# Kernel tuning notes

Measured on AMD Instinct MI355X. Metric: run time of the kernel, lower is better.

Reference implementation:

```python
import jax, jax.numpy as jnp
import numpy as np

ALPHA = 0.2  # leaky relu slope
NEG_BIG = -9e15


def setup_inputs() -> dict:
    key = jax.random.key(0)
    k1, k2, k3, k4 = jax.random.split(key, 4)
    B, N, Fin, Fout = 8, 2048, 128, 128
    h = jax.random.normal(k1, (B, N, Fin), dtype=jnp.float32)
    adj = jax.random.randint(k2, (N, N), 0, 2, dtype=jnp.int32)
    # xavier_uniform with gain=1.414
    limW = 1.414 * np.sqrt(6.0 / (Fin + Fout))
    W = jax.random.uniform(k3, (Fin, Fout), minval=-limW, maxval=limW, dtype=jnp.float32)
    lima = 1.414 * np.sqrt(6.0 / (2 * Fout + 1))
    a = jax.random.uniform(k4, (2 * Fout, 1), minval=-lima, maxval=lima, dtype=jnp.float32)
    return {"h": h, "adj": adj, "W": W, "a": a}


def reference(h, adj, W, a):
    # Wh: [B, N, F]
    Wh = jnp.einsum("bnf,fo->bno", h, W)
    Fout = W.shape[1]
    a1, a2 = a[:Fout, 0], a[Fout:, 0]  # [F], [F]
    # Additive score decomposition (same math as concat trick):
    # e[b,i,j] = leakyrelu(Wh_i . a1 + Wh_j . a2)
    s1 = Wh @ a1  # [B, N] (source/query part)
    s2 = Wh @ a2  # [B, N] (target part)
    e = s1[:, :, None] + s2[:, None, :]  # [B, N, N]
    e = jnp.where(e > 0, e, ALPHA * e)   # leaky relu
    e = jnp.where(adj[None, :, :] > 0, e, NEG_BIG)
    attention = jax.nn.softmax(e, axis=2)  # [B, N, N]
    # dropout is identity in eval mode
    h_prime = jnp.einsum("bij,bjf->bif", attention, Wh)
    return h_prime
```

## Files before the change

### kernel.cpp

```cpp
#include <hip/hip_runtime.h>
#include <hip/hip_bf16.h>
#include <stdint.h>

#define ALPHA 0.2f

typedef __attribute__((ext_vector_type(8))) short bf16x8;
typedef __attribute__((ext_vector_type(4))) float f32x4;

__device__ __forceinline__ short f2bf(float f) {
    union { float f; uint32_t u; } c; c.f = f;
    uint32_t u = c.u + 0x7FFF + ((c.u >> 16) & 1);
    return (short)(u >> 16);
}

__device__ __forceinline__ uint32_t pk_bf16(float lo, float hi) {
    union { float f; uint32_t u; } a, b;
    a.f = lo; b.f = hi;
    return __builtin_amdgcn_perm(b.u + 0x8000u, a.u + 0x8000u, 0x07060302u);
}

__device__ __forceinline__ void gload_lds16(const void* g, void* l) {
    __builtin_amdgcn_global_load_lds(
        (const __attribute__((address_space(1))) void*)g,
        (__attribute__((address_space(3))) void*)l, 16, 0, 0);
}

__global__ __launch_bounds__(256) void pack_adj_kernel(
        const int* __restrict__ adj, uint8_t* __restrict__ bytes,
        const float* __restrict__ W, short* __restrict__ WTg) {
    int t = blockIdx.x * 256 + threadIdx.x;
    const int4* a4 = reinterpret_cast<const int4*>(adj) + (size_t)t * 2;
    int4 x0 = a4[0], x1 = a4[1];
    uint32_t m = 0;
    m |= (x0.x > 0) ? 1u   : 0u;  m |= (x0.y > 0) ? 2u   : 0u;
    m |= (x0.z > 0) ? 4u   : 0u;  m |= (x0.w > 0) ? 8u   : 0u;
    m |= (x1.x > 0) ? 16u  : 0u;  m |= (x1.y > 0) ? 32u  : 0u;
    m |= (x1.z > 0) ? 64u  : 0u;  m |= (x1.w > 0) ? 128u : 0u;
    bytes[t] = (uint8_t)m;

    if (blockIdx.x < 64) {
        int idx = blockIdx.x * 256 + threadIdx.x;
        int k = idx >> 7, f = idx & 127;
        WTg[f * 128 + k] = f2bf(W[k * 128 + f]);
    }
}

__global__ __launch_bounds__(256) void wh_kernel(
        const float* __restrict__ h, const short* __restrict__ WTg,
        const float* __restrict__ a, short* __restrict__ whT,
        float* __restrict__ s1g, float* __restrict__ s2g) {
    __shared__ float sred[4][2][16];
    __shared__ short tr[4][32][24];

    int tid = threadIdx.x, wid = tid >> 6, lane = tid & 63;
    int q = lane >> 4, n = lane & 15;
    int bb = blockIdx.x & 7;
    int tile = blockIdx.x >> 3;
    int rb = bb * 2048 + tile * 16;
    int row = rb + n;

    f32x4 acc[2] = {};
    #pragma unroll
    for (int kc = 0; kc < 4; ++kc) {
        const float* hp = h + (size_t)row * 128 + kc * 32 + q * 8;
        float4 h0 = reinterpret_cast<const float4*>(hp)[0];
        float4 h1 = reinterpret_cast<const float4*>(hp)[1];
        bf16x8 afrag;
        afrag[0] = f2bf(h0.x); afrag[1] = f2bf(h0.y);
        afrag[2] = f2bf(h0.z); afrag[3] = f2bf(h0.w);
        afrag[4] = f2bf(h1.x); afrag[5] = f2bf(h1.y);
        afrag[6] = f2bf(h1.z); afrag[7] = f2bf(h1.w);
        #pragma unroll
        for (int u = 0; u < 2; ++u) {
            int t = wid * 2 + u;
            bf16x8 bfrag = *reinterpret_cast<const bf16x8*>(
                WTg + (t * 16 + n) * 128 + kc * 32 + q * 8);
            acc[u] = __builtin_amdgcn_mfma_f32_16x16x32_bf16(afrag, bfrag, acc[u], 0, 0, 0);
        }
    }

    float p1[4] = {0.f, 0.f, 0.f, 0.f}, p2[4] = {0.f, 0.f, 0.f, 0.f};
    #pragma unroll
    for (int u = 0; u < 2; ++u) {
        int c = (wid * 2 + u) * 16 + n;
        float a1c = a[c] * 1.442695041f;
        float a2c = a[128 + c] * 1.442695041f;
        #pragma unroll
        for (int r = 0; r < 4; ++r) {
            p1[r] += acc[u][r] * a1c;
            p2[r] += acc[u][r] * a2c;
        }
    }
    #pragma unroll
    for (int d = 1; d < 16; d <<= 1) {
        #pragma unroll
        for (int r = 0; r < 4; ++r) {
            p1[r] += __shfl_xor(p1[r], d);
            p2[r] += __shfl_xor(p2[r], d);
        }
    }
    if (n == 0) {
        #pragma unroll
        for (int r = 0; r < 4; ++r) {
            sred[wid][0][q * 4 + r] = p1[r];
            sred[wid][1][q * 4 + r] = p2[r];
        }
    }

    #pragma unroll
    for (int u = 0; u < 2; ++u)
        #pragma unroll
        for (int r = 0; r < 4; ++r)
            tr[wid][u * 16 + n][q * 4 + r] = f2bf(acc[u][r]);
    __syncthreads();

    if (wid == 0 && lane < 16) {
        float v1 = 0.f, v2 = 0.f;
        #pragma unroll
        for (int v = 0; v < 4; ++v) { v1 += sred[v][0][lane]; v2 += sred[v][1][lane]; }
        s1g[rb + lane] = v1;
        s2g[rb + lane] = v2;
    }

    int jr = rb & 2047;
    int fl = lane & 31, jh = lane >> 5;
    bf16x8 v = *reinterpret_cast<const bf16x8*>(&tr[wid][fl][jh * 8]);
    int f = wid * 32 + fl;
    int t = f >> 4, nn = f & 15;
    int jc = jr >> 5;
    int qg = ((jr & 31) >> 3) + jh;
    *reinterpret_cast<bf16x8*>(
        whT + (size_t)(bb * 64 + jc) * 4096 + t * 512 + qg * 128 + nn * 8) = v;
}

__global__ __launch_bounds__(256, 3) void attn_kernel(
        const short* __restrict__ whT, const float* __restrict__ s1g,
        const float* __restrict__ s2g, const uint8_t* __restrict__ adjb,
        float* __restrict__ out) {
    __shared__ char ring[2][2][8192];
    __shared__ uint32_t mlds[32 * 65];
    __shared__ float s2lds[2048];
    __shared__ float dslds[4][16];

    int tid = threadIdx.x, wid = tid >> 6, lane = tid & 63;
    int q = lane >> 4, n = lane & 15;
    int rg = wid & 1, jh = wid >> 1;
    int b  = blockIdx.x & 7;
    int ib = (blockIdx.x >> 3) * 32;
    int row = ib + rg * 16 + n;

    float s1A = s1g[b * 2048 + row];
    const char* gbase = reinterpret_cast<const char*>(whT) + (size_t)b * 524288;

    {
        int r = tid >> 3, sub = tid & 7;
        const uint4* src = reinterpret_cast<const uint4*>(
            adjb + (size_t)(ib + r) * 256 + sub * 32);
        uint4 v0 = src[0], v1 = src[1];
        uint32_t* dst = &mlds[r * 65 + sub * 8];
        dst[0] = v0.x; dst[1] = v0.y; dst[2] = v0.z; dst[3] = v0.w;
        dst[4] = v1.x; dst[5] = v1.y; dst[6] = v1.z; dst[7] = v1.w;
    }
    {
        const float* s2b = s2g + b * 2048;
        float4 v0 = *reinterpret_cast<const float4*>(s2b + tid * 8);
        float4 v1 = *reinterpret_cast<const float4*>(s2b + tid * 8 + 4);
        *reinterpret_cast<float4*>(&s2lds[tid * 8])     = v0;
        *reinterpret_cast<float4*>(&s2lds[tid * 8 + 4]) = v1;
    }

    {
        const char* g = gbase + (size_t)(jh * 32) * 8192 + rg * 4096 + lane * 16;
        char* l = &ring[jh][0][rg * 4096];
        #pragma unroll
        for (int i = 0; i < 4; ++i)
            gload_lds16(g + i * 1024, l + i * 1024);
    }
    __syncthreads();

    f32x4 acc[8] = {};
    float ds = 0.f;
    int mrow = (rg * 16 + n) * 65 + jh * 32;

    for (int c = 0; c < 32; ++c) {
        int cur = c & 1;
        if (c < 31) {
            const char* g = gbase + (size_t)(jh * 32 + c + 1) * 8192
                            + rg * 4096 + lane * 16;
            char* l = &ring[jh][cur ^ 1][rg * 4096];
            #pragma unroll
            for (int i = 0; i < 4; ++i)
                gload_lds16(g + i * 1024, l + i * 1024);
        }

        const char* cb = &ring[jh][cur][0] + lane * 16;
        bf16x8 nb[8];
        #pragma unroll
        for (int t = 0; t < 8; ++t)
            nb[t] = *reinterpret_cast<const bf16x8*>(cb + t * 1024);

        uint32_t mA = mlds[mrow + c] >> (q * 8);
        int sb = (jh * 32 + c) * 32 + q * 8;
        float4 s2a = *reinterpret_cast<const float4*>(&s2lds[sb]);
        float4 s2c = *reinterpret_cast<const float4*>(&s2lds[sb + 4]);
        float s2arr[8] = {s2a.x, s2a.y, s2a.z, s2a.w,
                          s2c.x, s2c.y, s2c.z, s2c.w};

        float p[8];
        #pragma unroll
        for (int j = 0; j < 8; ++j) {
            float e = s1A + s2arr[j];
            e = fmaxf(e, ALPHA * e);
            float v = ((mA >> j) & 1) ? __builtin_amdgcn_exp2f(e) : 0.0f;
            ds += v; p[j] = v;
        }
        union { uint32_t u32[4]; bf16x8 v; } cv;
        #pragma unroll
        for (int pp = 0; pp < 4; ++pp)
            cv.u32[pp] = pk_bf16(p[2 * pp], p[2 * pp + 1]);

        #pragma unroll
        for (int t = 0; t < 8; ++t)
            acc[t] = __builtin_amdgcn_mfma_f32_16x16x32_bf16(cv.v, nb[t], acc[t], 0, 0, 0);

        __syncthreads();
    }

    ds += __shfl_xor(ds, 16); ds += __shfl_xor(ds, 32);
    if (q == 0) dslds[wid][n] = ds;

    f32x4* cbuf = reinterpret_cast<f32x4*>(&ring[0][0][0]);
    __syncthreads();
    if (jh == 1) {
        #pragma unroll
        for (int i = 0; i < 8; ++i)
            cbuf[(rg * 8 + i) * 64 + lane] = acc[i];
    }
    __syncthreads();
    if (jh == 0) {
        #pragma unroll
        for (int i = 0; i < 8; ++i)
            acc[i] += cbuf[(rg * 8 + i) * 64 + lane];

        float dtot = dslds[rg][n] + dslds[2 + rg][n];
        float rd[4];
        #pragma unroll
        for (int r = 0; r < 4; ++r)
            rd[r] = 1.0f / __shfl(dtot, q * 4 + r);

        size_t ob = ((size_t)b * 2048 + ib + rg * 16) * 128;
        #pragma unroll
        for (int t = 0; t < 8; ++t)
            #pragma unroll
            for (int r = 0; r < 4; ++r)
                out[ob + (size_t)(q * 4 + r) * 128 + t * 16 + n] = acc[t][r] * rd[r];
    }
}

extern "C" void kernel_launch(void* const* d_in, const int* in_sizes, int n_in,
                              void* d_out, int out_size, void* d_ws, size_t ws_size,
                              hipStream_t stream) {
    const float* h   = (const float*)d_in[0];
    const int*   adj = (const int*)d_in[1];
    const float* W   = (const float*)d_in[2];
    const float* a   = (const float*)d_in[3];
    float* out = (float*)d_out;

    char* ws = (char*)d_ws;
    short* whT = (short*)ws;
    float* s1  = (float*)(ws + 4194304);
    float* s2  = (float*)(ws + 4259840);
    uint8_t* bytes = (uint8_t*)(ws + 4325376);

    short* WTg = (short*)d_out + (4194304 - 16384);

    pack_adj_kernel<<<2048, 256, 0, stream>>>(adj, bytes, W, WTg);
    wh_kernel<<<1024, 256, 0, stream>>>(h, WTg, a, whT, s1, s2);
    attn_kernel<<<512, 256, 0, stream>>>(whT, s1, s2, bytes, out);
}
```

Before: 108.2 us.

## Fuse pack, Wh and attention kernels into one cooperative kernel with grid syncs

Merges the three launches (adjacency packing, Wh projection, attention) into a single cooperative kernel of 512 blocks, using grid.sync between phases. Each block now does several pack passes and two Wh tiles, and shared memory is reused across phases through one raw buffer. The aim is to remove launch overhead and inter-kernel gaps. In exchange the attention phase drops from 3 to 2 blocks-per-CU occupancy hints, and it adds grid-wide barrier costs. WTg also moves from the output buffer to the workspace.

```diff
diff --git a/kernel.cpp b/kernel.cpp
--- a/kernel.cpp
+++ b/kernel.cpp
@@ -1,6 +1,9 @@
 #include <hip/hip_runtime.h>
 #include <hip/hip_bf16.h>
+#include <hip/hip_cooperative_groups.h>
 #include <stdint.h>
+
+namespace cg = cooperative_groups;
 
 #define ALPHA 0.2f
 
@@ -25,235 +28,251 @@
         (__attribute__((address_space(3))) void*)l, 16, 0, 0);
 }
 
-__global__ __launch_bounds__(256) void pack_adj_kernel(
-        const int* __restrict__ adj, uint8_t* __restrict__ bytes,
-        const float* __restrict__ W, short* __restrict__ WTg) {
-    int t = blockIdx.x * 256 + threadIdx.x;
-    const int4* a4 = reinterpret_cast<const int4*>(adj) + (size_t)t * 2;
-    int4 x0 = a4[0], x1 = a4[1];
-    uint32_t m = 0;
-    m |= (x0.x > 0) ? 1u   : 0u;  m |= (x0.y > 0) ? 2u   : 0u;
-    m |= (x0.z > 0) ? 4u   : 0u;  m |= (x0.w > 0) ? 8u   : 0u;
-    m |= (x1.x > 0) ? 16u  : 0u;  m |= (x1.y > 0) ? 32u  : 0u;
-    m |= (x1.z > 0) ? 64u  : 0u;  m |= (x1.w > 0) ? 128u : 0u;
-    bytes[t] = (uint8_t)m;
-
-    if (blockIdx.x < 64) {
-        int idx = blockIdx.x * 256 + threadIdx.x;
-        int k = idx >> 7, f = idx & 127;
-        WTg[f * 128 + k] = f2bf(W[k * 128 + f]);
-    }
-}
-
-__global__ __launch_bounds__(256) void wh_kernel(
-        const float* __restrict__ h, const short* __restrict__ WTg,
-        const float* __restrict__ a, short* __restrict__ whT,
-        float* __restrict__ s1g, float* __restrict__ s2g) {
-    __shared__ float sred[4][2][16];
-    __shared__ short tr[4][32][24];
+__global__ __launch_bounds__(256, 2) void fused_kernel(
+        const float* __restrict__ h, const int* __restrict__ adj,
+        const float* __restrict__ W, const float* __restrict__ a,
+        short* __restrict__ whT, float* __restrict__ s1g,
+        float* __restrict__ s2g, uint8_t* __restrict__ adjb,
+        short* __restrict__ WTg, float* __restrict__ out) {
+
+    __shared__ __align__(16) char smem[49536];
 
     int tid = threadIdx.x, wid = tid >> 6, lane = tid & 63;
     int q = lane >> 4, n = lane & 15;
-    int bb = blockIdx.x & 7;
-    int tile = blockIdx.x >> 3;
-    int rb = bb * 2048 + tile * 16;
-    int row = rb + n;
-
-    f32x4 acc[2] = {};
-    #pragma unroll
-    for (int kc = 0; kc < 4; ++kc) {
-        const float* hp = h + (size_t)row * 128 + kc * 32 + q * 8;
-        float4 h0 = reinterpret_cast<const float4*>(hp)[0];
-        float4 h1 = reinterpret_cast<const float4*>(hp)[1];
-        bf16x8 afrag;
-        afrag[0] = f2bf(h0.x); afrag[1] = f2bf(h0.y);
-        afrag[2] = f2bf(h0.z); afrag[3] = f2bf(h0.w);
-        afrag[4] = f2bf(h1.x); afrag[5] = f2bf(h1.y);
-        afrag[6] = f2bf(h1.z); afrag[7] = f2bf(h1.w);
+    cg::grid_group grid = cg::this_grid();
+
+    {
+        int gtid = blockIdx.x * 256 + tid;
         #pragma unroll
-        for (int u = 0; u < 2; ++u) {
-            int t = wid * 2 + u;
-            bf16x8 bfrag = *reinterpret_cast<const bf16x8*>(
-                WTg + (t * 16 + n) * 128 + kc * 32 + q * 8);
-            acc[u] = __builtin_amdgcn_mfma_f32_16x16x32_bf16(afrag, bfrag, acc[u], 0, 0, 0);
+        for (int pass = 0; pass < 4; ++pass) {
+            int t = pass * 131072 + gtid;
+            const int4* a4 = reinterpret_cast<const int4*>(adj) + (size_t)t * 2;
+            int4 x0 = a4[0], x1 = a4[1];
+            uint32_t m = 0;
+            m |= (x0.x > 0) ? 1u   : 0u;  m |= (x0.y > 0) ? 2u   : 0u;
+            m |= (x0.z > 0) ? 4u   : 0u;  m |= (x0.w > 0) ? 8u   : 0u;
+            m |= (x1.x > 0) ? 16u  : 0u;  m |= (x1.y > 0) ? 32u  : 0u;
+            m |= (x1.z > 0) ? 64u  : 0u;  m |= (x1.w > 0) ? 128u : 0u;
+            adjb[t] = (uint8_t)m;
+        }
+        if (blockIdx.x < 64) {
+            int idx = blockIdx.x * 256 + tid;
+            int k = idx >> 7, f = idx & 127;
+            WTg[f * 128 + k] = f2bf(W[k * 128 + f]);
         }
     }
 
-    float p1[4] = {0.f, 0.f, 0.f, 0.f}, p2[4] = {0.f, 0.f, 0.f, 0.f};
-    #pragma unroll
-    for (int u = 0; u < 2; ++u) {
-        int c = (wid * 2 + u) * 16 + n;
-        float a1c = a[c] * 1.442695041f;
-        float a2c = a[128 + c] * 1.442695041f;
+    __threadfence();
+    grid.sync();
+
+    {
+        float (*sred)[2][16] = reinterpret_cast<float (*)[2][16]>(smem);
+        short (*tr)[32][24]  = reinterpret_cast<short (*)[32][24]>(smem + 512);
+
+        int bb = blockIdx.x & 7;
+        int tile0 = blockIdx.x >> 3;
         #pragma unroll
-        for (int r = 0; r < 4; ++r) {
-            p1[r] += acc[u][r] * a1c;
-            p2[r] += acc[u][r] * a2c;
+        for (int t2 = 0; t2 < 2; ++t2) {
+            if (t2) __syncthreads();
+            int tile = tile0 + t2 * 64;
+            int rb = bb * 2048 + tile * 16;
+            int row = rb + n;
+
+            f32x4 acc[2] = {};
+            #pragma unroll
+            for (int kc = 0; kc < 4; ++kc) {
+                const float* hp = h + (size_t)row * 128 + kc * 32 + q * 8;
+                float4 h0 = reinterpret_cast<const float4*>(hp)[0];
+                float4 h1 = reinterpret_cast<const float4*>(hp)[1];
+                bf16x8 afrag;
+                afrag[0] = f2bf(h0.x); afrag[1] = f2bf(h0.y);
+                afrag[2] = f2bf(h0.z); afrag[3] = f2bf(h0.w);
+                afrag[4] = f2bf(h1.x); afrag[5] = f2bf(h1.y);
+                afrag[6] = f2bf(h1.z); afrag[7] = f2bf(h1.w);
+                #pragma unroll
+                for (int u = 0; u < 2; ++u) {
+                    int t = wid * 2 + u;
+                    bf16x8 bfrag = *reinterpret_cast<const bf16x8*>(
+                        WTg + (t * 16 + n) * 128 + kc * 32 + q * 8);
+                    acc[u] = __builtin_amdgcn_mfma_f32_16x16x32_bf16(afrag, bfrag, acc[u], 0, 0, 0);
+                }
+            }
+
+            float p1[4] = {0.f, 0.f, 0.f, 0.f}, p2[4] = {0.f, 0.f, 0.f, 0.f};
+            #pragma unroll
+            for (int u = 0; u < 2; ++u) {
+                int c = (wid * 2 + u) * 16 + n;
+                float a1c = a[c] * 1.442695041f;
+                float a2c = a[128 + c] * 1.442695041f;
+                #pragma unroll
+                for (int r = 0; r < 4; ++r) {
+                    p1[r] += acc[u][r] * a1c;
+                    p2[r] += acc[u][r] * a2c;
+                }
+            }
+            #pragma unroll
+            for (int d = 1; d < 16; d <<= 1) {
+                #pragma unroll
+                for (int r = 0; r < 4; ++r) {
+                    p1[r] += __shfl_xor(p1[r], d);
+                    p2[r] += __shfl_xor(p2[r], d);
+                }
+            }
+            if (n == 0) {
+                #pragma unroll
+                for (int r = 0; r < 4; ++r) {
+                    sred[wid][0][q * 4 + r] = p1[r];
+                    sred[wid][1][q * 4 + r] = p2[r];
+                }
+            }
+
+            #pragma unroll
+            for (int u = 0; u < 2; ++u)
+                #pragma unroll
+                for (int r = 0; r < 4; ++r)
+                    tr[wid][u * 16 + n][q * 4 + r] = f2bf(acc[u][r]);
+            __syncthreads();
+
+            if (wid == 0 && lane < 16) {
+                float v1 = 0.f, v2 = 0.f;
+                #pragma unroll
+                for (int v = 0; v < 4; ++v) { v1 += sred[v][0][lane]; v2 += sred[v][1][lane]; }
+                s1g[rb + lane] = v1;
+                s2g[rb + lane] = v2;
+            }
+
+            int jr = rb & 2047;
+            int fl = lane & 31, jh = lane >> 5;
+            bf16x8 v = *reinterpret_cast<const bf16x8*>(&tr[wid][fl][jh * 8]);
+            int f = wid * 32 + fl;
+            int t = f >> 4, nn = f & 15;
+            int jc = jr >> 5;
+            int qg = ((jr & 31) >> 3) + jh;
+            *reinterpret_cast<bf16x8*>(
+                whT + (size_t)(bb * 64 + jc) * 4096 + t * 512 + qg * 128 + nn * 8) = v;
         }
     }
-    #pragma unroll
-    for (int d = 1; d < 16; d <<= 1) {
-        #pragma unroll
-        for (int r = 0; r < 4; ++r) {
-            p1[r] += __shfl_xor(p1[r], d);
-            p2[r] += __shfl_xor(p2[r], d);
-        }
-    }
-    if (n == 0) {
-        #pragma unroll
-        for (int r = 0; r < 4; ++r) {
-            sred[wid][0][q * 4 + r] = p1[r];
-            sred[wid][1][q * 4 + r] = p2[r];
-        }
-    }
-
-    #pragma unroll
-    for (int u = 0; u < 2; ++u)
-        #pragma unroll
-        for (int r = 0; r < 4; ++r)
-            tr[wid][u * 16 + n][q * 4 + r] = f2bf(acc[u][r]);
-    __syncthreads();
-
-    if (wid == 0 && lane < 16) {
-        float v1 = 0.f, v2 = 0.f;
-        #pragma unroll
-        for (int v = 0; v < 4; ++v) { v1 += sred[v][0][lane]; v2 += sred[v][1][lane]; }
-        s1g[rb + lane] = v1;
-        s2g[rb + lane] = v2;
-    }
-
-    int jr = rb & 2047;
-    int fl = lane & 31, jh = lane >> 5;
-    bf16x8 v = *reinterpret_cast<const bf16x8*>(&tr[wid][fl][jh * 8]);
-    int f = wid * 32 + fl;
-    int t = f >> 4, nn = f & 15;
-    int jc = jr >> 5;
-    int qg = ((jr & 31) >> 3) + jh;
-    *reinterpret_cast<bf16x8*>(
-        whT + (size_t)(bb * 64 + jc) * 4096 + t * 512 + qg * 128 + nn * 8) = v;
-}
-
-__global__ __launch_bounds__(256, 3) void attn_kernel(
-        const short* __restrict__ whT, const float* __restrict__ s1g,
-        const float* __restrict__ s2g, const uint8_t* __restrict__ adjb,
-        float* __restrict__ out) {
-    __shared__ char ring[2][2][8192];
-    __shared__ uint32_t mlds[32 * 65];
-    __shared__ float s2lds[2048];
-    __shared__ float dslds[4][16];
-
-    int tid = threadIdx.x, wid = tid >> 6, lane = tid & 63;
-    int q = lane >> 4, n = lane & 15;
-    int rg = wid & 1, jh = wid >> 1;
-    int b  = blockIdx.x & 7;
-    int ib = (blockIdx.x >> 3) * 32;
-    int row = ib + rg * 16 + n;
-
-    float s1A = s1g[b * 2048 + row];
-    const char* gbase = reinterpret_cast<const char*>(whT) + (size_t)b * 524288;
+
+    __threadfence();
+    grid.sync();
 
     {
-        int r = tid >> 3, sub = tid & 7;
-        const uint4* src = reinterpret_cast<const uint4*>(
-            adjb + (size_t)(ib + r) * 256 + sub * 32);
-        uint4 v0 = src[0], v1 = src[1];
-        uint32_t* dst = &mlds[r * 65 + sub * 8];
-        dst[0] = v0.x; dst[1] = v0.y; dst[2] = v0.z; dst[3] = v0.w;
-        dst[4] = v1.x; dst[5] = v1.y; dst[6] = v1.z; dst[7] = v1.w;
-    }
-    {
-        const float* s2b = s2g + b * 2048;
-        float4 v0 = *reinterpret_cast<const float4*>(s2b + tid * 8);
-        float4 v1 = *reinterpret_cast<const float4*>(s2b + tid * 8 + 4);
-        *reinterpret_cast<float4*>(&s2lds[tid * 8])     = v0;
-        *reinterpret_cast<float4*>(&s2lds[tid * 8 + 4]) = v1;
-    }
-
-    {
-        const char* g = gbase + (size_t)(jh * 32) * 8192 + rg * 4096 + lane * 16;
-        char* l = &ring[jh][0][rg * 4096];
-        #pragma unroll
-        for (int i = 0; i < 4; ++i)
-            gload_lds16(g + i * 1024, l + i * 1024);
-    }
-    __syncthreads();
-
-    f32x4 acc[8] = {};
-    float ds = 0.f;
-    int mrow = (rg * 16 + n) * 65 + jh * 32;
-
-    for (int c = 0; c < 32; ++c) {
-        int cur = c & 1;
-        if (c < 31) {
-            const char* g = gbase + (size_t)(jh * 32 + c + 1) * 8192
-                            + rg * 4096 + lane * 16;
-            char* l = &ring[jh][cur ^ 1][rg * 4096];
+        char (*ring)[2][8192] = reinterpret_cast<char (*)[2][8192]>(smem);
+        uint32_t* mlds = reinterpret_cast<uint32_t*>(smem + 32768);
+        float* s2lds = reinterpret_cast<float*>(smem + 41088);
+        float (*dslds)[16] = reinterpret_cast<float (*)[16]>(smem + 49280);
+
+        int rg = wid & 1, jh = wid >> 1;
+        int b  = blockIdx.x & 7;
+        int ib = (blockIdx.x >> 3) * 32;
+        int row = ib + rg * 16 + n;
+
+        float s1A = s1g[b * 2048 + row];
+        const char* gbase = reinterpret_cast<const char*>(whT) + (size_t)b * 524288;
+
+        {
+            int r = tid >> 3, sub = tid & 7;
+            const uint4* src = reinterpret_cast<const uint4*>(
+                adjb + (size_t)(ib + r) * 256 + sub * 32);
+            uint4 v0 = src[0], v1 = src[1];
+            uint32_t* dst = &mlds[r * 65 + sub * 8];
+            dst[0] = v0.x; dst[1] = v0.y; dst[2] = v0.z; dst[3] = v0.w;
+            dst[4] = v1.x; dst[5] = v1.y; dst[6] = v1.z; dst[7] = v1.w;
+        }
+        {
+            const float* s2b = s2g + b * 2048;
+            float4 v0 = *reinterpret_cast<const float4*>(s2b + tid * 8);
+            float4 v1 = *reinterpret_cast<const float4*>(s2b + tid * 8 + 4);
+            *reinterpret_cast<float4*>(&s2lds[tid * 8])     = v0;
+            *reinterpret_cast<float4*>(&s2lds[tid * 8 + 4]) = v1;
+        }
+
+        {
+            const char* g = gbase + (size_t)(jh * 32) * 8192 + rg * 4096 + lane * 16;
+            char* l = &ring[jh][0][rg * 4096];
             #pragma unroll
             for (int i = 0; i < 4; ++i)
                 gload_lds16(g + i * 1024, l + i * 1024);
         }
-
-        const char* cb = &ring[jh][cur][0] + lane * 16;
-        bf16x8 nb[8];
-        #pragma unroll
-        for (int t = 0; t < 8; ++t)
-            nb[t] = *reinterpret_cast<const bf16x8*>(cb + t * 1024);
-
-        uint32_t mA = mlds[mrow + c] >> (q * 8);
-        int sb = (jh * 32 + c) * 32 + q * 8;
-        float4 s2a = *reinterpret_cast<const float4*>(&s2lds[sb]);
-        float4 s2c = *reinterpret_cast<const float4*>(&s2lds[sb + 4]);
-        float s2arr[8] = {s2a.x, s2a.y, s2a.z, s2a.w,
-                          s2c.x, s2c.y, s2c.z, s2c.w};
-
-        float p[8];
-        #pragma unroll
-        for (int j = 0; j < 8; ++j) {
-            float e = s1A + s2arr[j];
-            e = fmaxf(e, ALPHA * e);
-            float v = ((mA >> j) & 1) ? __builtin_amdgcn_exp2f(e) : 0.0f;
-            ds += v; p[j] = v;
-        }
-        union { uint32_t u32[4]; bf16x8 v; } cv;
-        #pragma unroll
-        for (int pp = 0; pp < 4; ++pp)
-            cv.u32[pp] = pk_bf16(p[2 * pp], p[2 * pp + 1]);
-
-        #pragma unroll
-        for (int t = 0; t < 8; ++t)
-            acc[t] = __builtin_amdgcn_mfma_f32_16x16x32_bf16(cv.v, nb[t], acc[t], 0, 0, 0);
-
         __syncthreads();
-    }
-
-    ds += __shfl_xor(ds, 16); ds += __shfl_xor(ds, 32);
-    if (q == 0) dslds[wid][n] = ds;
-
-    f32x4* cbuf = reinterpret_cast<f32x4*>(&ring[0][0][0]);
-    __syncthreads();
-    if (jh == 1) {
-        #pragma unroll
-        for (int i = 0; i < 8; ++i)
-            cbuf[(rg * 8 + i) * 64 + lane] = acc[i];
-    }
-    __syncthreads();
-    if (jh == 0) {
-        #pragma unroll
-        for (int i = 0; i < 8; ++i)
-            acc[i] += cbuf[(rg * 8 + i) * 64 + lane];
-
-        float dtot = dslds[rg][n] + dslds[2 + rg][n];
-        float rd[4];
-        #pragma unroll
-        for (int r = 0; r < 4; ++r)
-            rd[r] = 1.0f / __shfl(dtot, q * 4 + r);
-
-        size_t ob = ((size_t)b * 2048 + ib + rg * 16) * 128;
-        #pragma unroll
-        for (int t = 0; t < 8; ++t)
+
+        f32x4 acc[8] = {};
+        float ds = 0.f;
+        int mrow = (rg * 16 + n) * 65 + jh * 32;
+
+        for (int c = 0; c < 32; ++c) {
+            int cur = c & 1;
+            if (c < 31) {
+                const char* g = gbase + (size_t)(jh * 32 + c + 1) * 8192
+                                + rg * 4096 + lane * 16;
+                char* l = &ring[jh][cur ^ 1][rg * 4096];
+                #pragma unroll
+                for (int i = 0; i < 4; ++i)
+                    gload_lds16(g + i * 1024, l + i * 1024);
+            }
+
+            const char* cb = &ring[jh][cur][0] + lane * 16;
+            bf16x8 nb[8];
+            #pragma unroll
+            for (int t = 0; t < 8; ++t)
+                nb[t] = *reinterpret_cast<const bf16x8*>(cb + t * 1024);
+
+            uint32_t mA = mlds[mrow + c] >> (q * 8);
+            int sb = (jh * 32 + c) * 32 + q * 8;
+            float4 s2a = *reinterpret_cast<const float4*>(&s2lds[sb]);
+            float4 s2c = *reinterpret_cast<const float4*>(&s2lds[sb + 4]);
+            float s2arr[8] = {s2a.x, s2a.y, s2a.z, s2a.w,
+                              s2c.x, s2c.y, s2c.z, s2c.w};
+
+            float p[8];
+            #pragma unroll
+            for (int j = 0; j < 8; ++j) {
+                float e = s1A + s2arr[j];
+                e = fmaxf(e, ALPHA * e);
+                float v = ((mA >> j) & 1) ? __builtin_amdgcn_exp2f(e) : 0.0f;
+                ds += v; p[j] = v;
+            }
+            union { uint32_t u32[4]; bf16x8 v; } cv;
+            #pragma unroll
+            for (int pp = 0; pp < 4; ++pp)
+                cv.u32[pp] = pk_bf16(p[2 * pp], p[2 * pp + 1]);
+
+            #pragma unroll
+            for (int t = 0; t < 8; ++t)
+                acc[t] = __builtin_amdgcn_mfma_f32_16x16x32_bf16(cv.v, nb[t], acc[t], 0, 0, 0);
+
+            __syncthreads();
+        }
+
+        ds += __shfl_xor(ds, 16); ds += __shfl_xor(ds, 32);
+        if (q == 0) dslds[wid][n] = ds;
+
+        f32x4* cbuf = reinterpret_cast<f32x4*>(&ring[0][0][0]);
+        __syncthreads();
+        if (jh == 1) {
+            #pragma unroll
+            for (int i = 0; i < 8; ++i)
+                cbuf[(rg * 8 + i) * 64 + lane] = acc[i];
+        }
+        __syncthreads();
+        if (jh == 0) {
+            #pragma unroll
+            for (int i = 0; i < 8; ++i)
+                acc[i] += cbuf[(rg * 8 + i) * 64 + lane];
+
+            float dtot = dslds[rg][n] + dslds[2 + rg][n];
+            float rd[4];
             #pragma unroll
             for (int r = 0; r < 4; ++r)
-                out[ob + (size_t)(q * 4 + r) * 128 + t * 16 + n] = acc[t][r] * rd[r];
+                rd[r] = 1.0f / __shfl(dtot, q * 4 + r);
+
+            size_t ob = ((size_t)b * 2048 + ib + rg * 16) * 128;
+            #pragma unroll
+            for (int t = 0; t < 8; ++t)
+                #pragma unroll
+                for (int r = 0; r < 4; ++r)
+                    out[ob + (size_t)(q * 4 + r) * 128 + t * 16 + n] = acc[t][r] * rd[r];
+        }
     }
 }
 
@@ -271,10 +290,11 @@
     float* s1  = (float*)(ws + 4194304);
     float* s2  = (float*)(ws + 4259840);
     uint8_t* bytes = (uint8_t*)(ws + 4325376);
-
-    short* WTg = (short*)d_out + (4194304 - 16384);
-
-    pack_adj_kernel<<<2048, 256, 0, stream>>>(adj, bytes, W, WTg);
-    wh_kernel<<<1024, 256, 0, stream>>>(h, WTg, a, whT, s1, s2);
-    attn_kernel<<<512, 256, 0, stream>>>(whT, s1, s2, bytes, out);
-}
+    short* WTg = (short*)(ws + 4849664);
+
+    void* args[] = { (void*)&h, (void*)&adj, (void*)&W, (void*)&a,
+                     (void*)&whT, (void*)&s1, (void*)&s2, (void*)&bytes,
+                     (void*)&WTg, (void*)&out };
+    hipLaunchCooperativeKernel(reinterpret_cast<void*>(fused_kernel),
+                               dim3(512), dim3(256), args, 0, stream);
+}
```

Result: slower. 298.0 us (+175.5%).

## Replace LDS ring staging with register double-buffered direct global loads

Applied to the files above, without the earlier changes.

The attention loop no longer stages value tiles through a shared-memory ring with async global-to-LDS copies and a block barrier per chunk. Each wave now loads its MFMA operands straight from global memory into two alternating register sets, prefetching the next chunk while computing the current one. This removes per-iteration __syncthreads and LDS traffic, but doubles global/L2 reads (waves sharing a chunk each load it) and raises register use, with occupancy hint lowered from 3 to 2 blocks. The W transpose scratch is also moved from the output buffer into the workspace.

```diff
diff --git a/kernel.cpp b/kernel.cpp
--- a/kernel.cpp
+++ b/kernel.cpp
@@ -17,12 +17,6 @@
     union { float f; uint32_t u; } a, b;
     a.f = lo; b.f = hi;
     return __builtin_amdgcn_perm(b.u + 0x8000u, a.u + 0x8000u, 0x07060302u);
-}
-
-__device__ __forceinline__ void gload_lds16(const void* g, void* l) {
-    __builtin_amdgcn_global_load_lds(
-        (const __attribute__((address_space(1))) void*)g,
-        (__attribute__((address_space(3))) void*)l, 16, 0, 0);
 }
 
 __global__ __launch_bounds__(256) void pack_adj_kernel(
@@ -133,14 +127,22 @@
         whT + (size_t)(bb * 64 + jc) * 4096 + t * 512 + qg * 128 + nn * 8) = v;
 }
 
-__global__ __launch_bounds__(256, 3) void attn_kernel(
+__device__ __forceinline__ void load_nb(const char* gb, int chunk, int lane,
+                                        bf16x8* nb) {
+    const char* cb = gb + (size_t)chunk * 8192 + lane * 16;
+    #pragma unroll
+    for (int t = 0; t < 8; ++t)
+        nb[t] = *reinterpret_cast<const bf16x8*>(cb + t * 1024);
+}
+
+__global__ __launch_bounds__(256, 2) void attn_kernel(
         const short* __restrict__ whT, const float* __restrict__ s1g,
         const float* __restrict__ s2g, const uint8_t* __restrict__ adjb,
         float* __restrict__ out) {
-    __shared__ char ring[2][2][8192];
     __shared__ uint32_t mlds[32 * 65];
     __shared__ float s2lds[2048];
     __shared__ float dslds[4][16];
+    __shared__ f32x4 cbuf[1024];
 
     int tid = threadIdx.x, wid = tid >> 6, lane = tid & 63;
     int q = lane >> 4, n = lane & 15;
@@ -168,68 +170,76 @@
         *reinterpret_cast<float4*>(&s2lds[tid * 8])     = v0;
         *reinterpret_cast<float4*>(&s2lds[tid * 8 + 4]) = v1;
     }
-
-    {
-        const char* g = gbase + (size_t)(jh * 32) * 8192 + rg * 4096 + lane * 16;
-        char* l = &ring[jh][0][rg * 4096];
-        #pragma unroll
-        for (int i = 0; i < 4; ++i)
-            gload_lds16(g + i * 1024, l + i * 1024);
-    }
     __syncthreads();
 
     f32x4 acc[8] = {};
     float ds = 0.f;
     int mrow = (rg * 16 + n) * 65 + jh * 32;
-
-    for (int c = 0; c < 32; ++c) {
-        int cur = c & 1;
-        if (c < 31) {
-            const char* g = gbase + (size_t)(jh * 32 + c + 1) * 8192
-                            + rg * 4096 + lane * 16;
-            char* l = &ring[jh][cur ^ 1][rg * 4096];
-            #pragma unroll
-            for (int i = 0; i < 4; ++i)
-                gload_lds16(g + i * 1024, l + i * 1024);
-        }
-
-        const char* cb = &ring[jh][cur][0] + lane * 16;
-        bf16x8 nb[8];
-        #pragma unroll
-        for (int t = 0; t < 8; ++t)
-            nb[t] = *reinterpret_cast<const bf16x8*>(cb + t * 1024);
-
-        uint32_t mA = mlds[mrow + c] >> (q * 8);
-        int sb = (jh * 32 + c) * 32 + q * 8;
-        float4 s2a = *reinterpret_cast<const float4*>(&s2lds[sb]);
-        float4 s2c = *reinterpret_cast<const float4*>(&s2lds[sb + 4]);
-        float s2arr[8] = {s2a.x, s2a.y, s2a.z, s2a.w,
-                          s2c.x, s2c.y, s2c.z, s2c.w};
-
-        float p[8];
-        #pragma unroll
-        for (int j = 0; j < 8; ++j) {
-            float e = s1A + s2arr[j];
-            e = fmaxf(e, ALPHA * e);
-            float v = ((mA >> j) & 1) ? __builtin_amdgcn_exp2f(e) : 0.0f;
-            ds += v; p[j] = v;
-        }
-        union { uint32_t u32[4]; bf16x8 v; } cv;
-        #pragma unroll
-        for (int pp = 0; pp < 4; ++pp)
-            cv.u32[pp] = pk_bf16(p[2 * pp], p[2 * pp + 1]);
-
-        #pragma unroll
-        for (int t = 0; t < 8; ++t)
-            acc[t] = __builtin_amdgcn_mfma_f32_16x16x32_bf16(cv.v, nb[t], acc[t], 0, 0, 0);
-
-        __syncthreads();
+    int cb0 = jh * 32;
+
+    bf16x8 nbA[8], nbB[8];
+    load_nb(gbase, cb0, lane, nbA);
+
+    #pragma unroll 1
+    for (int cc = 0; cc < 32; cc += 2) {
+        load_nb(gbase, cb0 + cc + 1, lane, nbB);
+
+        {
+            int c = cc;
+            uint32_t mA = mlds[mrow + c] >> (q * 8);
+            int sb = (cb0 + c) * 32 + q * 8;
+            float4 s2a = *reinterpret_cast<const float4*>(&s2lds[sb]);
+            float4 s2c = *reinterpret_cast<const float4*>(&s2lds[sb + 4]);
+            float s2arr[8] = {s2a.x, s2a.y, s2a.z, s2a.w,
+                              s2c.x, s2c.y, s2c.z, s2c.w};
+            float p[8];
+            #pragma unroll
+            for (int j = 0; j < 8; ++j) {
+                float e = s1A + s2arr[j];
+                e = fmaxf(e, ALPHA * e);
+                float v = ((mA >> j) & 1) ? __builtin_amdgcn_exp2f(e) : 0.0f;
+                ds += v; p[j] = v;
+            }
+            union { uint32_t u32[4]; bf16x8 v; } cv;
+            #pragma unroll
+            for (int pp = 0; pp < 4; ++pp)
+                cv.u32[pp] = pk_bf16(p[2 * pp], p[2 * pp + 1]);
+            #pragma unroll
+            for (int t = 0; t < 8; ++t)
+                acc[t] = __builtin_amdgcn_mfma_f32_16x16x32_bf16(cv.v, nbA[t], acc[t], 0, 0, 0);
+        }
+
+        if (cc + 2 < 32) load_nb(gbase, cb0 + cc + 2, lane, nbA);
+
+        {
+            int c = cc + 1;
+            uint32_t mA = mlds[mrow + c] >> (q * 8);
+            int sb = (cb0 + c) * 32 + q * 8;
+            float4 s2a = *reinterpret_cast<const float4*>(&s2lds[sb]);
+            float4 s2c = *reinterpret_cast<const float4*>(&s2lds[sb + 4]);
+            float s2arr[8] = {s2a.x, s2a.y, s2a.z, s2a.w,
+                              s2c.x, s2c.y, s2c.z, s2c.w};
+            float p[8];
+            #pragma unroll
+            for (int j = 0; j < 8; ++j) {
+                float e = s1A + s2arr[j];
+                e = fmaxf(e, ALPHA * e);
+                float v = ((mA >> j) & 1) ? __builtin_amdgcn_exp2f(e) : 0.0f;
+                ds += v; p[j] = v;
+            }
+            union { uint32_t u32[4]; bf16x8 v; } cv;
+            #pragma unroll
+            for (int pp = 0; pp < 4; ++pp)
+                cv.u32[pp] = pk_bf16(p[2 * pp], p[2 * pp + 1]);
+            #pragma unroll
+            for (int t = 0; t < 8; ++t)
+                acc[t] = __builtin_amdgcn_mfma_f32_16x16x32_bf16(cv.v, nbB[t], acc[t], 0, 0, 0);
+        }
     }
 
     ds += __shfl_xor(ds, 16); ds += __shfl_xor(ds, 32);
     if (q == 0) dslds[wid][n] = ds;
 
-    f32x4* cbuf = reinterpret_cast<f32x4*>(&ring[0][0][0]);
     __syncthreads();
     if (jh == 1) {
         #pragma unroll
@@ -271,8 +281,7 @@
     float* s1  = (float*)(ws + 4194304);
     float* s2  = (float*)(ws + 4259840);
     uint8_t* bytes = (uint8_t*)(ws + 4325376);
-
-    short* WTg = (short*)d_out + (4194304 - 16384);
+    short* WTg = (short*)(ws + 4849664);
 
     pack_adj_kernel<<<2048, 256, 0, stream>>>(adj, bytes, W, WTg);
     wh_kernel<<<1024, 256, 0, stream>>>(h, WTg, a, whT, s1, s2);
```

Measured after the change: 105.6 us. 1.02x faster.
